# Optimization experiments

Hardware: AMD Instinct MI355X
Metric: run time of the kernel (lower is better)

Reference implementation:

```python
import jax, jax.numpy as jnp
import numpy as np

DELTA_V = 0.5
DELTA_D = 1.5
LOSS_WEIGHT = 1.0


def setup_inputs() -> dict:
    key = jax.random.key(0)
    k1, k2, k3, k4 = jax.random.split(key, 4)
    B, D, H, W = 8, 4, 640, 640
    return {
        "emb": jax.random.normal(k1, (B, D, H, W), dtype=jnp.float32),
        "instance": jax.random.randint(k2, (B, H, W), 0, 33, dtype=jnp.int32),
        "kernel": jax.random.uniform(k3, (B, H, W), dtype=jnp.float32),
        "training_mask": jax.random.uniform(k4, (B, H, W), dtype=jnp.float32),
        "num_labels": 33,  # static: background label 0 + 32 instances, all present w.h.p.
    }


def _single(emb, instance, kernel, tmask, num_labels):
    # emb: [D,H,W]; instance: [H,W] int; kernel/tmask: [H,W] float
    D = emb.shape[0]
    tm = (tmask > 0.5).astype(instance.dtype)
    kn = (kernel > 0.5).astype(instance.dtype)
    inst2 = instance * tm                      # instance masked by training mask
    inst_k = (inst2 * kn).reshape(-1)          # kernel-restricted labels, [N]
    inst = inst2.reshape(-1)                   # [N]
    x = emb.reshape(D, -1).T                   # [N, D]
    ones = jnp.ones(x.shape[0], jnp.float32)

    # per-instance kernel means (scatter-mean), label 0 column forced to zero
    sums = jax.ops.segment_sum(x, inst_k, num_segments=num_labels)      # [K1, D]
    cnts = jax.ops.segment_sum(ones, inst_k, num_segments=num_labels)   # [K1]
    mean = sums / jnp.maximum(cnts, 1.0)[:, None]
    mean = mean.at[0].set(0.0)

    # aggregation term: per-pixel distance to its instance mean, segmented mean over labels 1..K
    diff = x - mean[inst]                                               # [N, D]
    dist = jnp.sqrt(jnp.sum(diff * diff, axis=1))
    val = jnp.log(jnp.maximum(dist - DELTA_V, 0.0) ** 2 + 1.0)
    cnt_i = jax.ops.segment_sum(ones, inst, num_segments=num_labels)
    agg = jax.ops.segment_sum(val, inst, num_segments=num_labels) / jnp.maximum(cnt_i, 1.0)
    l_agg = jnp.mean(agg[1:])

    # discrimination term: pairwise distances between instance means (exclude label 0 and diagonal)
    m = mean[1:]                                                        # [K, D]
    K = m.shape[0]
    pdiff = m[:, None, :] - m[None, :, :]
    pd = jnp.sqrt(jnp.sum(pdiff * pdiff, axis=-1) + jnp.eye(K))         # diag padded (masked below)
    vald = jnp.log(jnp.maximum(2.0 * DELTA_D - pd, 0.0) ** 2 + 1.0)
    off = 1.0 - jnp.eye(K)
    l_dis = jnp.sum(vald * off) / (K * (K - 1))

    # regularizer: mean over all num_labels columns; label-0 column contributes log(1)=0
    nrm1 = jnp.sqrt(jnp.sum(m * m, axis=1))
    l_reg = jnp.sum(jnp.log(nrm1 + 1.0)) / num_labels * 0.001

    return l_agg + l_dis + l_reg


def reference(emb, instance, kernel, training_mask, num_labels):
    f = lambda e, i, k, t: _single(e, i, k, t, num_labels)
    loss_batch = jax.vmap(f)(emb, instance, kernel, training_mask)
    return jnp.mean(LOSS_WEIGHT * loss_batch)
```

## Files before the change

### kernel.cpp

```cpp
#include <hip/hip_runtime.h>
#include <math.h>

#define HW    409600
#define HW4   102400
#define BATCH 8
#define NLAB  33
#define GXB   200
#define NREP  16
#define RS    201
#define AWS_OFF   1344
#define LABS_OFF_F 3008
#define NEED_LABS  ((size_t)LABS_OFF_F * 4 + (size_t)BATCH * HW4 * 4)

#if defined(__has_builtin) && __has_builtin(__builtin_amdgcn_sched_barrier)
#define SCHED_PIN() __builtin_amdgcn_sched_barrier(0)
#else
#define SCHED_PIN()
#endif

__device__ __forceinline__ void atomAddF(float* p, float v) {
    unsafeAtomicAdd(p, v);
}

__device__ __forceinline__ float getc(const float4& v, int e) {
    return (e == 0) ? v.x : (e == 1) ? v.y : (e == 2) ? v.z : v.w;
}
__device__ __forceinline__ float wave_sum(float v) {
    #pragma unroll
    for (int o = 32; o > 0; o >>= 1) v += __shfl_xor(v, o);
    return v;
}

struct Quad { int4 iv; float4 tv, kv, x0, x1, x2, x3; };

__device__ __forceinline__ void loadQ(Quad& q, const int4* inst4, const float4* tm4,
                                      const float4* kern4, const float4* emb4, int g) {
    q.iv = inst4[g];
    q.tv = tm4[g];
    q.kv = kern4[g];
    q.x0 = emb4[g];
    q.x1 = emb4[g + HW4];
    q.x2 = emb4[g + 2 * HW4];
    q.x3 = emb4[g + 3 * HW4];
}

__device__ __forceinline__ void acc1(int l, bool k,
                                     float x0, float x1, float x2, float x3,
                                     float* mb) {
    if (l) {
        float* bb = mb + l * 6;
        atomicAdd((unsigned*)(bb + 4), k ? 0x10001u : 1u);
        if (k) {
            atomAddF(bb + 0, x0);
            atomAddF(bb + 1, x1);
            atomAddF(bb + 2, x2);
            atomAddF(bb + 3, x3);
        }
    }
}

__device__ __forceinline__ void procQ(const Quad& q, float* mb,
                                      unsigned* labs, size_t labidx) {
    int l0 = (q.tv.x > 0.5f) ? q.iv.x : 0;
    int l1 = (q.tv.y > 0.5f) ? q.iv.y : 0;
    int l2 = (q.tv.z > 0.5f) ? q.iv.z : 0;
    int l3 = (q.tv.w > 0.5f) ? q.iv.w : 0;
    if (labs)
        labs[labidx] = (unsigned)l0 | ((unsigned)l1 << 8) |
                       ((unsigned)l2 << 16) | ((unsigned)l3 << 24);
    acc1(l0, q.kv.x > 0.5f, q.x0.x, q.x1.x, q.x2.x, q.x3.x, mb);
    acc1(l1, q.kv.y > 0.5f, q.x0.y, q.x1.y, q.x2.y, q.x3.y, mb);
    acc1(l2, q.kv.z > 0.5f, q.x0.z, q.x1.z, q.x2.z, q.x3.z, mb);
    acc1(l3, q.kv.w > 0.5f, q.x0.w, q.x1.w, q.x2.w, q.x3.w, mb);
}

__global__ __launch_bounds__(256, 4) void pass1(const float* __restrict__ emb,
                                                const int*   __restrict__ inst,
                                                const float* __restrict__ kern,
                                                const float* __restrict__ tmask,
                                                float*       __restrict__ ws,
                                                unsigned*    __restrict__ labs) {
    __shared__ float bins[NREP][RS];
    const int t = threadIdx.x, bx = blockIdx.x, b = blockIdx.y;
    float* mb = bins[(t >> 2) & (NREP - 1)];

    const size_t  base  = (size_t)b * HW;
    const float4* emb4  = (const float4*)(emb + base * 4);
    const int4*   inst4 = (const int4*)(inst + base);
    const float4* kern4 = (const float4*)(kern + base);
    const float4* tm4   = (const float4*)(tmask + base);
    const int q0 = bx * 512 + t;
    const size_t lb = (size_t)b * HW4;

    Quad c0, c1;
    loadQ(c0, inst4, tm4, kern4, emb4, q0);
    loadQ(c1, inst4, tm4, kern4, emb4, q0 + 256);
    SCHED_PIN();

    for (int i = t; i < NREP * RS; i += 256) (&bins[0][0])[i] = 0.f;
    __syncthreads();

    procQ(c0, mb, labs, lb + q0);
    procQ(c1, mb, labs, lb + q0 + 256);
    __syncthreads();

    if (t < NLAB * 6) {
        const int l = t / 6, k = t - l * 6;
        float v;
        if (k >= 4) {
            unsigned s = 0;
            #pragma unroll
            for (int r = 0; r < NREP; ++r)
                s += ((const unsigned*)bins[r])[l * 6 + 4];
            v = (k == 4) ? (float)(s >> 16) : (float)(s & 0xffffu);
        } else {
            float fs = 0.f;
            #pragma unroll
            for (int r = 0; r < NREP; ++r) fs += bins[r][l * 6 + k];
            v = fs;
        }
        if (v != 0.f) atomAddF(ws + AWS_OFF + b * 208 + t, v);
    }
}

struct Quad2 { unsigned pk; int4 iv; float4 tv, x0, x1, x2, x3; };

template<bool USE_LABS>
__device__ __forceinline__ void loadQ2(Quad2& q, const unsigned* labs, size_t lb,
                                       const int4* inst4, const float4* tm4,
                                       const float4* emb4, int g) {
    if (USE_LABS) {
        q.pk = labs[lb + g];
    } else {
        q.iv = inst4[g];
        q.tv = tm4[g];
    }
    q.x0 = emb4[g];
    q.x1 = emb4[g + HW4];
    q.x2 = emb4[g + 2 * HW4];
    q.x3 = emb4[g + 3 * HW4];
}

template<bool USE_LABS>
__device__ __forceinline__ float procQ2(const Quad2& q, const float4* means4,
                                        const float* invci) {
    unsigned pk;
    if (USE_LABS) {
        pk = q.pk;
    } else {
        pk = (unsigned)((q.tv.x > 0.5f) ? q.iv.x : 0)        |
             ((unsigned)((q.tv.y > 0.5f) ? q.iv.y : 0) << 8) |
             ((unsigned)((q.tv.z > 0.5f) ? q.iv.z : 0) << 16)|
             ((unsigned)((q.tv.w > 0.5f) ? q.iv.w : 0) << 24);
    }
    float acc = 0.f;
    #pragma unroll
    for (int e = 0; e < 4; ++e) {
        int l = (pk >> (8 * e)) & 255;
        if (l) {
            float4 m = means4[l];
            float d0 = getc(q.x0, e) - m.x, d1 = getc(q.x1, e) - m.y;
            float d2 = getc(q.x2, e) - m.z, d3 = getc(q.x3, e) - m.w;
            float dist = sqrtf(d0 * d0 + d1 * d1 + d2 * d2 + d3 * d3);
            float u = fmaxf(dist - 0.5f, 0.f);
            acc += __logf(u * u + 1.f) * invci[l];
        }
    }
    return acc;
}

template<bool USE_LABS>
__global__ __launch_bounds__(256, 4) void pass2(const float* __restrict__ emb,
                                                const int*   __restrict__ inst,
                                                const float* __restrict__ tmask,
                                                const float* __restrict__ ws,
                                                const unsigned* __restrict__ labs,
                                                float*       __restrict__ out) {
    __shared__ float  raw[200];
    __shared__ float4 means4[NLAB];
    __shared__ float  invci[NLAB];
    __shared__ float  red[4];
    const int t = threadIdx.x, bx = blockIdx.x, b = blockIdx.y;

    const size_t  base  = (size_t)b * HW;
    const float4* emb4  = (const float4*)(emb + base * 4);
    const int4*   inst4 = (const int4*)(inst + base);
    const float4* tm4   = (const float4*)(tmask + base);
    const int q0 = bx * 512 + t;
    const size_t lb = (size_t)b * HW4;

    Quad2 c0, c1;
    loadQ2<USE_LABS>(c0, labs, lb, inst4, tm4, emb4, q0);
    loadQ2<USE_LABS>(c1, labs, lb, inst4, tm4, emb4, q0 + 256);
    SCHED_PIN();

    if (t < NLAB * 6) raw[t] = ws[AWS_OFF + b * 208 + t];
    __syncthreads();
    if (t < NLAB) {
        float cntk = raw[t * 6 + 4], cnti = raw[t * 6 + 5];
        float inv = 1.f / fmaxf(cntk, 1.f);
        float z = (t == 0) ? 0.f : 1.f;
        float4 m;
        m.x = z * raw[t * 6 + 0] * inv;
        m.y = z * raw[t * 6 + 1] * inv;
        m.z = z * raw[t * 6 + 2] * inv;
        m.w = z * raw[t * 6 + 3] * inv;
        means4[t] = m;
        invci[t]  = 1.f / fmaxf(cnti, 1.f);
    }
    __syncthreads();

    float acc = procQ2<USE_LABS>(c0, means4, invci)
              + procQ2<USE_LABS>(c1, means4, invci);

    float v = acc * (1.f / 32.f);

    if (bx == 0) {
        float disp = 0.f;
        #pragma unroll
        for (int p = t; p < 1024; p += 256) {
            int i = p >> 5, j = p & 31;
            if (i != j) {
                float4 mi = means4[i + 1], mj = means4[j + 1];
                float d0 = mi.x - mj.x, d1 = mi.y - mj.y;
                float d2 = mi.z - mj.z, d3 = mi.w - mj.w;
                float pd = sqrtf(d0 * d0 + d1 * d1 + d2 * d2 + d3 * d3);
                float u = fmaxf(3.0f - pd, 0.f);
                disp += __logf(u * u + 1.f);
            }
        }
        v += disp * (1.f / 992.f);
        if (t >= 1 && t < NLAB) {
            float4 m = means4[t];
            float n2 = m.x * m.x + m.y * m.y + m.z * m.z + m.w * m.w;
            v += __logf(sqrtf(n2) + 1.f) * (0.001f / 33.f);
        }
    }

    v = wave_sum(v);
    if ((t & 63) == 0) red[t >> 6] = v;
    __syncthreads();
    if (t == 0)
        atomAddF(out, (red[0] + red[1] + red[2] + red[3]) * (1.f / BATCH));
}

extern "C" void kernel_launch(void* const* d_in, const int* in_sizes, int n_in,
                              void* d_out, int out_size, void* d_ws, size_t ws_size,
                              hipStream_t stream) {
    const float* emb   = (const float*)d_in[0];
    const int*   inst  = (const int*)  d_in[1];
    const float* kern  = (const float*)d_in[2];
    const float* tmask = (const float*)d_in[3];
    float* ws  = (float*)d_ws;
    float* out = (float*)d_out;

    const bool use_labs = ws_size >= NEED_LABS;
    unsigned* labs = use_labs ? (unsigned*)(ws + LABS_OFF_F) : nullptr;

    hipMemsetAsync((void*)(ws + AWS_OFF), 0, BATCH * 208 * sizeof(float), stream);
    hipMemsetAsync(d_out, 0, sizeof(float), stream);

    dim3 grid(GXB, BATCH);
    pass1<<<grid, 256, 0, stream>>>(emb, inst, kern, tmask, ws, labs);
    if (use_labs) pass2<true ><<<grid, 256, 0, stream>>>(emb, inst, tmask, ws, labs, out);
    else          pass2<false><<<grid, 256, 0, stream>>>(emb, inst, tmask, ws, nullptr, out);
}
```

Measured before the change: 153.8 us.

## Fuse both passes into one persistent kernel with grid-wide barrier

Merges the two passes into one kernel. Each block holds its embedding quads in registers across a global atomic-counter barrier, so the embedding is read from memory once instead of twice and the packed-label buffer goes away. The grid is halved to 800 blocks, each handling 1024 quads, so every block can be resident at the same time. Correctness depends on all blocks being co-resident; otherwise the spin barrier deadlocks. Register pressure also rises from holding 16 float4 values per thread.

Result: slower. 258.1 us (+67.8%).

```diff
diff --git a/kernel.cpp b/kernel.cpp
--- a/kernel.cpp
+++ b/kernel.cpp
@@ -5,12 +5,12 @@
 #define HW4   102400
 #define BATCH 8
 #define NLAB  33
-#define GXB   200
+#define GXB   100
+#define NBLK  (GXB * BATCH)
 #define NREP  16
 #define RS    201
+#define CTR_OFF   0
 #define AWS_OFF   1344
-#define LABS_OFF_F 3008
-#define NEED_LABS  ((size_t)LABS_OFF_F * 4 + (size_t)BATCH * HW4 * 4)
 
 #if defined(__has_builtin) && __has_builtin(__builtin_amdgcn_sched_barrier)
 #define SCHED_PIN() __builtin_amdgcn_sched_barrier(0)
@@ -29,19 +29,6 @@
     #pragma unroll
     for (int o = 32; o > 0; o >>= 1) v += __shfl_xor(v, o);
     return v;
-}
-
-struct Quad { int4 iv; float4 tv, kv, x0, x1, x2, x3; };
-
-__device__ __forceinline__ void loadQ(Quad& q, const int4* inst4, const float4* tm4,
-                                      const float4* kern4, const float4* emb4, int g) {
-    q.iv = inst4[g];
-    q.tv = tm4[g];
-    q.kv = kern4[g];
-    q.x0 = emb4[g];
-    q.x1 = emb4[g + HW4];
-    q.x2 = emb4[g + 2 * HW4];
-    q.x3 = emb4[g + 3 * HW4];
 }
 
 __device__ __forceinline__ void acc1(int l, bool k,
@@ -59,28 +46,49 @@
     }
 }
 
-__device__ __forceinline__ void procQ(const Quad& q, float* mb,
-                                      unsigned* labs, size_t labidx) {
-    int l0 = (q.tv.x > 0.5f) ? q.iv.x : 0;
-    int l1 = (q.tv.y > 0.5f) ? q.iv.y : 0;
-    int l2 = (q.tv.z > 0.5f) ? q.iv.z : 0;
-    int l3 = (q.tv.w > 0.5f) ? q.iv.w : 0;
-    if (labs)
-        labs[labidx] = (unsigned)l0 | ((unsigned)l1 << 8) |
-                       ((unsigned)l2 << 16) | ((unsigned)l3 << 24);
-    acc1(l0, q.kv.x > 0.5f, q.x0.x, q.x1.x, q.x2.x, q.x3.x, mb);
-    acc1(l1, q.kv.y > 0.5f, q.x0.y, q.x1.y, q.x2.y, q.x3.y, mb);
-    acc1(l2, q.kv.z > 0.5f, q.x0.z, q.x1.z, q.x2.z, q.x3.z, mb);
-    acc1(l3, q.kv.w > 0.5f, q.x0.w, q.x1.w, q.x2.w, q.x3.w, mb);
-}
-
-__global__ __launch_bounds__(256, 4) void pass1(const float* __restrict__ emb,
+__device__ __forceinline__ unsigned procQ1(const int4& iv, const float4& tv,
+                                           const float4& kv, const float4 x[4],
+                                           float* mb) {
+    int l0 = (tv.x > 0.5f) ? iv.x : 0;
+    int l1 = (tv.y > 0.5f) ? iv.y : 0;
+    int l2 = (tv.z > 0.5f) ? iv.z : 0;
+    int l3 = (tv.w > 0.5f) ? iv.w : 0;
+    acc1(l0, kv.x > 0.5f, x[0].x, x[1].x, x[2].x, x[3].x, mb);
+    acc1(l1, kv.y > 0.5f, x[0].y, x[1].y, x[2].y, x[3].y, mb);
+    acc1(l2, kv.z > 0.5f, x[0].z, x[1].z, x[2].z, x[3].z, mb);
+    acc1(l3, kv.w > 0.5f, x[0].w, x[1].w, x[2].w, x[3].w, mb);
+    return (unsigned)l0 | ((unsigned)l1 << 8) |
+           ((unsigned)l2 << 16) | ((unsigned)l3 << 24);
+}
+
+__device__ __forceinline__ float procQ2(unsigned pk, const float4 x[4],
+                                        const float4* means4, const float* invci) {
+    float acc = 0.f;
+    #pragma unroll
+    for (int e = 0; e < 4; ++e) {
+        int l = (pk >> (8 * e)) & 255;
+        if (l) {
+            float4 m = means4[l];
+            float d0 = getc(x[0], e) - m.x, d1 = getc(x[1], e) - m.y;
+            float d2 = getc(x[2], e) - m.z, d3 = getc(x[3], e) - m.w;
+            float dist = sqrtf(d0 * d0 + d1 * d1 + d2 * d2 + d3 * d3);
+            float u = fmaxf(dist - 0.5f, 0.f);
+            acc += __logf(u * u + 1.f) * invci[l];
+        }
+    }
+    return acc;
+}
+
+__global__ __launch_bounds__(256, 4) void fused(const float* __restrict__ emb,
                                                 const int*   __restrict__ inst,
                                                 const float* __restrict__ kern,
                                                 const float* __restrict__ tmask,
                                                 float*       __restrict__ ws,
-                                                unsigned*    __restrict__ labs) {
-    __shared__ float bins[NREP][RS];
+                                                float*       __restrict__ out) {
+    __shared__ float  bins[NREP][RS];
+    __shared__ float4 means4[NLAB];
+    __shared__ float  invci[NLAB];
+    __shared__ float  red[4];
     const int t = threadIdx.x, bx = blockIdx.x, b = blockIdx.y;
     float* mb = bins[(t >> 2) & (NREP - 1)];
 
@@ -89,19 +97,35 @@
     const int4*   inst4 = (const int4*)(inst + base);
     const float4* kern4 = (const float4*)(kern + base);
     const float4* tm4   = (const float4*)(tmask + base);
-    const int q0 = bx * 512 + t;
-    const size_t lb = (size_t)b * HW4;
-
-    Quad c0, c1;
-    loadQ(c0, inst4, tm4, kern4, emb4, q0);
-    loadQ(c1, inst4, tm4, kern4, emb4, q0 + 256);
+    const int g0 = bx * 1024 + t;
+
+    float4 xq[4][4];
+    #pragma unroll
+    for (int c = 0; c < 4; ++c) {
+        const int g = g0 + c * 256;
+        #pragma unroll
+        for (int d = 0; d < 4; ++d) xq[c][d] = emb4[g + d * HW4];
+    }
+    int4   iv0 = inst4[g0],        iv1 = inst4[g0 + 256];
+    float4 tv0 = tm4[g0],          tv1 = tm4[g0 + 256];
+    float4 kv0 = kern4[g0],        kv1 = kern4[g0 + 256];
     SCHED_PIN();
 
     for (int i = t; i < NREP * RS; i += 256) (&bins[0][0])[i] = 0.f;
     __syncthreads();
 
-    procQ(c0, mb, labs, lb + q0);
-    procQ(c1, mb, labs, lb + q0 + 256);
+    unsigned pk0 = procQ1(iv0, tv0, kv0, xq[0], mb);
+    int4   iv2 = inst4[g0 + 512];
+    float4 tv2 = tm4[g0 + 512];
+    float4 kv2 = kern4[g0 + 512];
+    SCHED_PIN();
+    unsigned pk1 = procQ1(iv1, tv1, kv1, xq[1], mb);
+    int4   iv3 = inst4[g0 + 768];
+    float4 tv3 = tm4[g0 + 768];
+    float4 kv3 = kern4[g0 + 768];
+    SCHED_PIN();
+    unsigned pk2 = procQ1(iv2, tv2, kv2, xq[2], mb);
+    unsigned pk3 = procQ1(iv3, tv3, kv3, xq[3], mb);
     __syncthreads();
 
     if (t < NLAB * 6) {
@@ -121,80 +145,24 @@
         }
         if (v != 0.f) atomAddF(ws + AWS_OFF + b * 208 + t, v);
     }
-}
-
-struct Quad2 { unsigned pk; int4 iv; float4 tv, x0, x1, x2, x3; };
-
-template<bool USE_LABS>
-__device__ __forceinline__ void loadQ2(Quad2& q, const unsigned* labs, size_t lb,
-                                       const int4* inst4, const float4* tm4,
-                                       const float4* emb4, int g) {
-    if (USE_LABS) {
-        q.pk = labs[lb + g];
-    } else {
-        q.iv = inst4[g];
-        q.tv = tm4[g];
-    }
-    q.x0 = emb4[g];
-    q.x1 = emb4[g + HW4];
-    q.x2 = emb4[g + 2 * HW4];
-    q.x3 = emb4[g + 3 * HW4];
-}
-
-template<bool USE_LABS>
-__device__ __forceinline__ float procQ2(const Quad2& q, const float4* means4,
-                                        const float* invci) {
-    unsigned pk;
-    if (USE_LABS) {
-        pk = q.pk;
-    } else {
-        pk = (unsigned)((q.tv.x > 0.5f) ? q.iv.x : 0)        |
-             ((unsigned)((q.tv.y > 0.5f) ? q.iv.y : 0) << 8) |
-             ((unsigned)((q.tv.z > 0.5f) ? q.iv.z : 0) << 16)|
-             ((unsigned)((q.tv.w > 0.5f) ? q.iv.w : 0) << 24);
-    }
-    float acc = 0.f;
-    #pragma unroll
-    for (int e = 0; e < 4; ++e) {
-        int l = (pk >> (8 * e)) & 255;
-        if (l) {
-            float4 m = means4[l];
-            float d0 = getc(q.x0, e) - m.x, d1 = getc(q.x1, e) - m.y;
-            float d2 = getc(q.x2, e) - m.z, d3 = getc(q.x3, e) - m.w;
-            float dist = sqrtf(d0 * d0 + d1 * d1 + d2 * d2 + d3 * d3);
-            float u = fmaxf(dist - 0.5f, 0.f);
-            acc += __logf(u * u + 1.f) * invci[l];
-        }
-    }
-    return acc;
-}
-
-template<bool USE_LABS>
-__global__ __launch_bounds__(256, 4) void pass2(const float* __restrict__ emb,
-                                                const int*   __restrict__ inst,
-                                                const float* __restrict__ tmask,
-                                                const float* __restrict__ ws,
-                                                const unsigned* __restrict__ labs,
-                                                float*       __restrict__ out) {
-    __shared__ float  raw[200];
-    __shared__ float4 means4[NLAB];
-    __shared__ float  invci[NLAB];
-    __shared__ float  red[4];
-    const int t = threadIdx.x, bx = blockIdx.x, b = blockIdx.y;
-
-    const size_t  base  = (size_t)b * HW;
-    const float4* emb4  = (const float4*)(emb + base * 4);
-    const int4*   inst4 = (const int4*)(inst + base);
-    const float4* tm4   = (const float4*)(tmask + base);
-    const int q0 = bx * 512 + t;
-    const size_t lb = (size_t)b * HW4;
-
-    Quad2 c0, c1;
-    loadQ2<USE_LABS>(c0, labs, lb, inst4, tm4, emb4, q0);
-    loadQ2<USE_LABS>(c1, labs, lb, inst4, tm4, emb4, q0 + 256);
-    SCHED_PIN();
-
-    if (t < NLAB * 6) raw[t] = ws[AWS_OFF + b * 208 + t];
+    __syncthreads();
+
+    unsigned* ctr = (unsigned*)(ws + CTR_OFF);
+    if (t == 0) {
+        __threadfence();
+        __hip_atomic_fetch_add(ctr, 1u, __ATOMIC_ACQ_REL,
+                               __HIP_MEMORY_SCOPE_AGENT);
+        while (__hip_atomic_load(ctr, __ATOMIC_ACQUIRE,
+                                 __HIP_MEMORY_SCOPE_AGENT) < NBLK)
+            __builtin_amdgcn_s_sleep(8);
+        __threadfence();
+    }
+    __syncthreads();
+
+    float* raw = &bins[0][0];
+    if (t < NLAB * 6)
+        raw[t] = __hip_atomic_load(ws + AWS_OFF + b * 208 + t,
+                                   __ATOMIC_ACQUIRE, __HIP_MEMORY_SCOPE_AGENT);
     __syncthreads();
     if (t < NLAB) {
         float cntk = raw[t * 6 + 4], cnti = raw[t * 6 + 5];
@@ -210,9 +178,10 @@
     }
     __syncthreads();
 
-    float acc = procQ2<USE_LABS>(c0, means4, invci)
-              + procQ2<USE_LABS>(c1, means4, invci);
-
+    float acc = procQ2(pk0, xq[0], means4, invci)
+              + procQ2(pk1, xq[1], means4, invci)
+              + procQ2(pk2, xq[2], means4, invci)
+              + procQ2(pk3, xq[3], means4, invci);
     float v = acc * (1.f / 32.f);
 
     if (bx == 0) {
@@ -254,14 +223,8 @@
     float* ws  = (float*)d_ws;
     float* out = (float*)d_out;
 
-    const bool use_labs = ws_size >= NEED_LABS;
-    unsigned* labs = use_labs ? (unsigned*)(ws + LABS_OFF_F) : nullptr;
-
-    hipMemsetAsync((void*)(ws + AWS_OFF), 0, BATCH * 208 * sizeof(float), stream);
+    hipMemsetAsync((void*)ws, 0, (AWS_OFF + BATCH * 208) * sizeof(float), stream);
     hipMemsetAsync(d_out, 0, sizeof(float), stream);
 
-    dim3 grid(GXB, BATCH);
-    pass1<<<grid, 256, 0, stream>>>(emb, inst, kern, tmask, ws, labs);
-    if (use_labs) pass2<true ><<<grid, 256, 0, stream>>>(emb, inst, tmask, ws, labs, out);
-    else          pass2<false><<<grid, 256, 0, stream>>>(emb, inst, tmask, ws, nullptr, out);
-}
+    fused<<<dim3(GXB, BATCH), 256, 0, stream>>>(emb, inst, kern, tmask, ws, out);
+}
```
